# Performance work log

Measured on AMD Instinct MI355X. Metric: run time of the kernel, lower is better.

The kernel has to match this reference:

```python
import jax, jax.numpy as jnp
import numpy as np

B, L, D, H, I = 4, 1024, 2048, 16, 8192
DH = D // H  # 128
EPS = 1e-6


def setup_inputs() -> dict:
    key = jax.random.key(0)
    ks = jax.random.split(key, 10)
    hidden_states = jax.random.normal(ks[0], (B, L, D), dtype=jnp.float32)
    # additive causal mask [B,1,L,L]: 0 on allowed, large negative on masked
    causal = jnp.tril(jnp.ones((L, L), dtype=bool))
    attention_mask = jnp.where(causal, 0.0, -1e9).astype(jnp.float32)
    attention_mask = jnp.broadcast_to(attention_mask[None, None], (B, 1, L, L))
    # RoPE tables [B,L,DH]
    inv_freq = 1.0 / (10000.0 ** (jnp.arange(0, DH, 2, dtype=jnp.float32) / DH))
    pos = jnp.arange(L, dtype=jnp.float32)
    freqs = pos[:, None] * inv_freq[None, :]            # [L, DH/2]
    emb = jnp.concatenate([freqs, freqs], axis=-1)       # [L, DH]
    cos = jnp.broadcast_to(jnp.cos(emb)[None], (B, L, DH)).astype(jnp.float32)
    sin = jnp.broadcast_to(jnp.sin(emb)[None], (B, L, DH)).astype(jnp.float32)
    s = 0.02
    return {
        "hidden_states": hidden_states,
        "attention_mask": attention_mask,
        "cos": cos,
        "sin": sin,
        "q_w": jax.random.normal(ks[1], (D, D), jnp.float32) * s,
        "k_w": jax.random.normal(ks[2], (D, D), jnp.float32) * s,
        "v_w": jax.random.normal(ks[3], (D, D), jnp.float32) * s,
        "o_w": jax.random.normal(ks[4], (D, D), jnp.float32) * s,
        "gate_w": jax.random.normal(ks[5], (I, D), jnp.float32) * s,
        "up_w": jax.random.normal(ks[6], (I, D), jnp.float32) * s,
        "down_w": jax.random.normal(ks[7], (D, I), jnp.float32) * s,
        "ln1_w": jnp.ones((D,), jnp.float32),
        "ln2_w": jnp.ones((D,), jnp.float32),
    }


def _rms_norm(x, w):
    var = jnp.mean(jnp.square(x), axis=-1, keepdims=True)
    return x * jax.lax.rsqrt(var + EPS) * w


def _rotate_half(x):
    x1, x2 = jnp.split(x, 2, axis=-1)
    return jnp.concatenate([-x2, x1], axis=-1)


def reference(hidden_states, attention_mask, cos, sin, q_w, k_w, v_w, o_w,
              gate_w, up_w, down_w, ln1_w, ln2_w):
    residual = hidden_states
    h = _rms_norm(hidden_states, ln1_w)                       # [B,L,D]
    # QKV projections (torch Linear: x @ W^T)
    def heads(x, w):
        return (x @ w.T).reshape(B, L, H, DH).transpose(0, 2, 1, 3)  # [B,H,L,DH]
    q, k, v = heads(h, q_w), heads(h, k_w), heads(h, v_w)
    cos_b, sin_b = cos[:, None], sin[:, None]                 # [B,1,L,DH]
    q = q * cos_b + _rotate_half(q) * sin_b
    k = k * cos_b + _rotate_half(k) * sin_b
    scores = jnp.einsum('bhqd,bhkd->bhqk', q, k) / jnp.sqrt(jnp.float32(DH))
    scores = scores + attention_mask                          # [B,H,L,L]
    attn = jax.nn.softmax(scores, axis=-1)
    ctx = jnp.einsum('bhqk,bhkd->bhqd', attn, v)              # [B,H,L,DH]
    ctx = ctx.transpose(0, 2, 1, 3).reshape(B, L, D)
    attn_out = ctx @ o_w.T
    h1 = residual + attn_out
    h2 = _rms_norm(h1, ln2_w)
    mlp = (jax.nn.silu(h2 @ gate_w.T) * (h2 @ up_w.T)) @ down_w.T
    out = h1 + mlp
    return out, attn
```

## Files before the change

kernel.cpp:

```cpp
#include <hip/hip_runtime.h>


typedef __bf16 bf16;
typedef __bf16 bf16x8 __attribute__((ext_vector_type(8)));
typedef __bf16 bf16x4 __attribute__((ext_vector_type(4)));
typedef float  f32x4  __attribute__((ext_vector_type(4)));

constexpr int   kB  = 4;
constexpr int   kL  = 1024;
constexpr int   kD  = 2048;
constexpr int   kH  = 16;
constexpr int   kI  = 8192;
constexpr int   kDH = 128;
constexpr int   kQKV = 3 * kD;
constexpr float kEps = 1e-6f;
constexpr float kScoreScale = 0.08838834764831845f;

typedef __attribute__((address_space(1))) void gvoid_t;
typedef __attribute__((address_space(3))) void lvoid_t;

__device__ __forceinline__ void gload_lds16(const void* g, void* l) {
  __builtin_amdgcn_global_load_lds((gvoid_t*)g, (lvoid_t*)l, 16, 0, 0);
}

#define ASM_VMCNT(n) asm volatile("s_waitcnt vmcnt(" #n ")" ::: "memory")

__device__ __forceinline__ void bar_raw() {
  asm volatile("" ::: "memory");
  __builtin_amdgcn_s_barrier();
  asm volatile("" ::: "memory");
}

__global__ __launch_bounds__(256) void cast_f32_bf16_kernel(
    const float* __restrict__ x, bf16* __restrict__ y, long n) {
  long i = ((long)blockIdx.x * 256 + threadIdx.x) * 4;
  long stride = (long)gridDim.x * 256 * 4;
  for (; i < n; i += stride) {
    const float4 v = *reinterpret_cast<const float4*>(x + i);
    bf16x4 o;
    o[0] = (bf16)v.x; o[1] = (bf16)v.y; o[2] = (bf16)v.z; o[3] = (bf16)v.w;
    *reinterpret_cast<bf16x4*>(y + i) = o;
  }
}

__global__ __launch_bounds__(256) void add_inplace_kernel(
    float* __restrict__ o, const float* __restrict__ p, long n) {
  long i = ((long)blockIdx.x * 256 + threadIdx.x) * 4;
  const long stride = (long)gridDim.x * 1024;
  for (; i < n; i += stride) {
    float4 a = *(float4*)(o + i);
    const float4 b = *(const float4*)(p + i);
    a.x += b.x; a.y += b.y; a.z += b.z; a.w += b.w;
    *(float4*)(o + i) = a;
  }
}

__global__ __launch_bounds__(256) void rmsnorm_kernel(
    const float* __restrict__ x, const float* __restrict__ w,
    bf16* __restrict__ out) {
  const long row = blockIdx.x;
  const float* xr = x + row * (long)kD;
  bf16* orow = out + row * (long)kD;
  const int t = threadIdx.x;

  float4 v0 = *(const float4*)(xr + t * 8);
  float4 v1 = *(const float4*)(xr + t * 8 + 4);
  float ss = v0.x * v0.x + v0.y * v0.y + v0.z * v0.z + v0.w * v0.w +
             v1.x * v1.x + v1.y * v1.y + v1.z * v1.z + v1.w * v1.w;

  __shared__ float red[4];
  for (int off = 32; off > 0; off >>= 1) ss += __shfl_down(ss, off);
  if ((t & 63) == 0) red[t >> 6] = ss;
  __syncthreads();
  const float tot = red[0] + red[1] + red[2] + red[3];
  const float rs = rsqrtf(tot / (float)kD + kEps);

  float4 w0 = *(const float4*)(w + t * 8);
  float4 w1 = *(const float4*)(w + t * 8 + 4);
  bf16x8 o;
  o[0] = (bf16)(v0.x * rs * w0.x); o[1] = (bf16)(v0.y * rs * w0.y);
  o[2] = (bf16)(v0.z * rs * w0.z); o[3] = (bf16)(v0.w * rs * w0.w);
  o[4] = (bf16)(v1.x * rs * w1.x); o[5] = (bf16)(v1.y * rs * w1.y);
  o[6] = (bf16)(v1.z * rs * w1.z); o[7] = (bf16)(v1.w * rs * w1.w);
  *(bf16x8*)(orow + t * 8) = o;
}

__global__ __launch_bounds__(256) void rope_kernel(
    bf16* __restrict__ qkv, const float* __restrict__ cosb,
    const float* __restrict__ sinb) {
  const long row = blockIdx.x;
  const float* cr = cosb + row * (long)kDH;
  const float* sr = sinb + row * (long)kDH;
  bf16* qr = qkv + row * (long)kQKV;
  bf16* kr = qr + kD;
  const int t = threadIdx.x;
#pragma unroll
  for (int it = 0; it < 4; ++it) {
    const int p = it * 256 + t;
    const int h = p >> 6, i = p & 63;
    const int i0 = h * kDH + i, i1 = i0 + 64;
    const float c0 = cr[i], s0 = sr[i], c1 = cr[i + 64], s1 = sr[i + 64];
    const float q0 = (float)qr[i0], q1 = (float)qr[i1];
    qr[i0] = (bf16)(q0 * c0 - q1 * s0);
    qr[i1] = (bf16)(q1 * c1 + q0 * s1);
    const float k0 = (float)kr[i0], k1 = (float)kr[i1];
    kr[i0] = (bf16)(k0 * c0 - k1 * s0);
    kr[i1] = (bf16)(k1 * c1 + k0 * s1);
  }
}

__global__ __launch_bounds__(256) void transpose_v_kernel(
    const bf16* __restrict__ qkv, bf16* __restrict__ vT) {
  __shared__ bf16 tile[32][33];
  const int z = blockIdx.z, b = z / kH, h = z % kH;
  const bf16* src = qkv + (long)b * kL * kQKV + 2 * kD + h * kDH;
  bf16* dst = vT + (long)z * kDH * kL;
  const int l0 = blockIdx.x * 32, d0 = blockIdx.y * 32;
  const int tx = threadIdx.x & 31, ty = threadIdx.x >> 5;
  for (int r = ty; r < 32; r += 8)
    tile[r][tx] = src[(long)(l0 + r) * kQKV + d0 + tx];
  __syncthreads();
  for (int r = ty; r < 32; r += 8)
    dst[(long)(d0 + r) * kL + l0 + tx] = tile[tx][r];
}

__global__ __launch_bounds__(256) void merge_stats_kernel(
    const float2* __restrict__ sp, float2* __restrict__ sm) {
  const int idx = blockIdx.x * 256 + threadIdx.x;
  const int row = idx & 1023;
  const int n = ((row >> 7) + 1) * 2;
  const float2* p = sp + ((long)idx << 4);
  float M = -3.0e38f;
  for (int i = 0; i < n; ++i) M = fmaxf(M, p[i].x);
  float S = 0.f;
  for (int i = 0; i < n; ++i) S += p[i].y * expf(p[i].x - M);
  sm[idx] = make_float2(M, 1.0f / S);
}

template <int EPI>
__global__ __launch_bounds__(512) void gemm8p(
    const bf16* __restrict__ A, int lda, const bf16* __restrict__ B, int ldb,
    bf16* __restrict__ C, int ldc, const bf16* __restrict__ Ep, int lde,
    int K) {
  __shared__ __align__(16) bf16 ls[2][2][2][128 * 64];
  const int t = threadIdx.x;
  const int m0 = blockIdx.x * 256, n0 = blockIdx.y * 256;
  const int wave = t >> 6, lane = t & 63;
  const int ah = wave >> 2;
  const int wm = ah * 128;
  const int wn = (wave & 3) * 64;
  const int bh = wn >> 7;
  const int wnr = wn & 127;
  const int lr = lane & 15, lg = lane >> 4;

  f32x4 acc[8][4] = {};

  auto stageHalf = [&](int b, int O, int h, int k0) {
    const bf16* S = O ? B : A;
    const int ld = O ? ldb : lda;
    const int base = O ? n0 : m0;
#pragma unroll
    for (int cc = 0; cc < 2; ++cc) {
      const int id = cc * 512 + t;
      const int row = id >> 3, cS = id & 7;
      const int cG = cS ^ (row & 7);
      gload_lds16(S + (long)(base + h * 128 + row) * ld + k0 + cG * 8,
                  (char*)&ls[b][O][h][0] + id * 16);
    }
  };

  auto lread = [&](int b, int O, int h, int row, int c16) {
    return *(const bf16x8*)((const char*)&ls[b][O][h][0] + row * 128 +
                            ((c16 ^ (row & 7)) << 4));
  };

  const int T = K >> 6;
  stageHalf(0, 0, 0, 0); stageHalf(0, 0, 1, 0);
  stageHalf(0, 1, 0, 0); stageHalf(0, 1, 1, 0);
  stageHalf(1, 1, 0, 64); stageHalf(1, 1, 1, 64);

  bf16x8 bfr[2][4];

  for (int w = 0; w < T; ++w) {
    const int c = w & 1;
    const int k1 = (w + 1) << 6, k2 = (w + 2) << 6;
#pragma unroll
    for (int p = 0; p < 4; ++p) {
      bf16x8 af[2][2];
      if (p == 0) {
        if (w + 1 < T) { ASM_VMCNT(4); } else { ASM_VMCNT(0); }
        bar_raw();
#pragma unroll
        for (int kk = 0; kk < 2; ++kk)
#pragma unroll
          for (int nf = 0; nf < 4; ++nf)
            bfr[kk][nf] = lread(c, 1, bh, wnr + nf * 16 + lr, kk * 4 + lg);
      }
#pragma unroll
      for (int kk = 0; kk < 2; ++kk)
#pragma unroll
        for (int mf = 0; mf < 2; ++mf)
          af[kk][mf] = lread(c, 0, ah, (2 * p + mf) * 16 + lr, kk * 4 + lg);
      if (p == 0 && w + 1 < T) stageHalf(c ^ 1, 0, 0, k1);
      if (p == 1 && w + 1 < T) stageHalf(c ^ 1, 0, 1, k1);
      if (p == 2 && w + 2 < T) stageHalf(c, 1, 0, k2);
      if (p == 3 && w + 2 < T) stageHalf(c, 1, 1, k2);
      bar_raw();
      asm volatile("s_waitcnt lgkmcnt(0)" ::: "memory");
      __builtin_amdgcn_sched_barrier(0);
      __builtin_amdgcn_s_setprio(1);
#pragma unroll
      for (int kk = 0; kk < 2; ++kk)
#pragma unroll
        for (int mf = 0; mf < 2; ++mf)
#pragma unroll
          for (int nf = 0; nf < 4; ++nf)
            acc[2 * p + mf][nf] = __builtin_amdgcn_mfma_f32_16x16x32_bf16(
                af[kk][mf], bfr[kk][nf], acc[2 * p + mf][nf], 0, 0, 0);
      __builtin_amdgcn_s_setprio(0);
      bar_raw();
    }
  }

#pragma unroll
  for (int mf = 0; mf < 8; ++mf) {
#pragma unroll
    for (int nf = 0; nf < 4; ++nf) {
      const int col = n0 + wn + nf * 16 + lr;
#pragma unroll
      for (int r = 0; r < 4; ++r) {
        const int row = m0 + wm + mf * 16 + lg * 4 + r;
        float val = acc[mf][nf][r];
        if constexpr (EPI == 3) {
          const float g = (float)Ep[(long)row * lde + col];
          val = (g / (1.0f + expf(-g))) * val;
        }
        C[(long)row * ldc + col] = (bf16)val;
      }
    }
  }
}

__global__ __launch_bounds__(512) void gemm8pF(
    const bf16* __restrict__ A, int lda, const bf16* __restrict__ B, int ldb,
    float* __restrict__ C, int ldc, float* __restrict__ Part, int K) {
  __shared__ __align__(16) bf16 ls[2][2][2][128 * 64];
  const int t = threadIdx.x;
  const int m0 = blockIdx.x * 256, n0 = blockIdx.y * 256;
  const long ko = (long)blockIdx.z * K;
  A += ko; B += ko;
  const int wave = t >> 6, lane = t & 63;
  const int ah = wave >> 2;
  const int wm = ah * 128;
  const int wn = (wave & 3) * 64;
  const int bh = wn >> 7;
  const int wnr = wn & 127;
  const int lr = lane & 15, lg = lane >> 4;

  f32x4 acc[8][4] = {};

  auto stageHalf = [&](int b, int O, int h, int k0) {
    const bf16* S = O ? B : A;
    const int ld = O ? ldb : lda;
    const int base = O ? n0 : m0;
#pragma unroll
    for (int cc = 0; cc < 2; ++cc) {
      const int id = cc * 512 + t;
      const int row = id >> 3, cS = id & 7;
      const int cG = cS ^ (row & 7);
      gload_lds16(S + (long)(base + h * 128 + row) * ld + k0 + cG * 8,
                  (char*)&ls[b][O][h][0] + id * 16);
    }
  };
  auto lread = [&](int b, int O, int h, int row, int c16) {
    return *(const bf16x8*)((const char*)&ls[b][O][h][0] + row * 128 +
                            ((c16 ^ (row & 7)) << 4));
  };

  const int T = K >> 6;
  stageHalf(0, 0, 0, 0); stageHalf(0, 0, 1, 0);
  stageHalf(0, 1, 0, 0); stageHalf(0, 1, 1, 0);
  stageHalf(1, 1, 0, 64); stageHalf(1, 1, 1, 64);

  bf16x8 bfr[2][4];
  for (int w = 0; w < T; ++w) {
    const int c = w & 1;
    const int k1 = (w + 1) << 6, k2 = (w + 2) << 6;
#pragma unroll
    for (int p = 0; p < 4; ++p) {
      bf16x8 af[2][2];
      if (p == 0) {
        if (w + 1 < T) { ASM_VMCNT(4); } else { ASM_VMCNT(0); }
        bar_raw();
#pragma unroll
        for (int kk = 0; kk < 2; ++kk)
#pragma unroll
          for (int nf = 0; nf < 4; ++nf)
            bfr[kk][nf] = lread(c, 1, bh, wnr + nf * 16 + lr, kk * 4 + lg);
      }
#pragma unroll
      for (int kk = 0; kk < 2; ++kk)
#pragma unroll
        for (int mf = 0; mf < 2; ++mf)
          af[kk][mf] = lread(c, 0, ah, (2 * p + mf) * 16 + lr, kk * 4 + lg);
      if (p == 0 && w + 1 < T) stageHalf(c ^ 1, 0, 0, k1);
      if (p == 1 && w + 1 < T) stageHalf(c ^ 1, 0, 1, k1);
      if (p == 2 && w + 2 < T) stageHalf(c, 1, 0, k2);
      if (p == 3 && w + 2 < T) stageHalf(c, 1, 1, k2);
      bar_raw();
      asm volatile("s_waitcnt lgkmcnt(0)" ::: "memory");
      __builtin_amdgcn_sched_barrier(0);
      __builtin_amdgcn_s_setprio(1);
#pragma unroll
      for (int kk = 0; kk < 2; ++kk)
#pragma unroll
        for (int mf = 0; mf < 2; ++mf)
#pragma unroll
          for (int nf = 0; nf < 4; ++nf)
            acc[2 * p + mf][nf] = __builtin_amdgcn_mfma_f32_16x16x32_bf16(
                af[kk][mf], bfr[kk][nf], acc[2 * p + mf][nf], 0, 0, 0);
      __builtin_amdgcn_s_setprio(0);
      bar_raw();
    }
  }

  const bool z0 = (blockIdx.z == 0);
#pragma unroll
  for (int mf = 0; mf < 8; ++mf) {
#pragma unroll
    for (int nf = 0; nf < 4; ++nf) {
      const int col = n0 + wn + nf * 16 + lr;
#pragma unroll
      for (int r = 0; r < 4; ++r) {
        const int row = m0 + wm + mf * 16 + lg * 4 + r;
        const long idx = (long)row * ldc + col;
        if (z0) C[idx] = acc[mf][nf][r] + C[idx];
        else    Part[idx] = acc[mf][nf][r];
      }
    }
  }
}

template <int EPIF>
__global__ __launch_bounds__(512) void gemm8pN128(
    const bf16* __restrict__ A, int lda, const bf16* __restrict__ B, int ldb,
    float* __restrict__ C, int ldc, const float* __restrict__ Ef, int lde,
    int K) {
  __shared__ __align__(16) bf16 lsA[2][2][128 * 64];
  __shared__ __align__(16) bf16 lsB[2][128 * 64];
  const int t = threadIdx.x;
  const int m0 = blockIdx.x * 256, n0 = blockIdx.y * 128;
  const int wave = t >> 6, lane = t & 63;
  const int ah = wave >> 2;
  const int wm = ah * 128;
  const int wn = (wave & 3) * 32;
  const int lr = lane & 15, lg = lane >> 4;

  f32x4 acc[8][2] = {};

  auto stageA = [&](int b, int h, int k0) {
#pragma unroll
    for (int cc = 0; cc < 2; ++cc) {
      const int id = cc * 512 + t;
      const int row = id >> 3, cS = id & 7;
      const int cG = cS ^ (row & 7);
      gload_lds16(A + (long)(m0 + h * 128 + row) * lda + k0 + cG * 8,
                  (char*)&lsA[b][h][0] + id * 16);
    }
  };
  auto stageB = [&](int b, int k0) {
#pragma unroll
    for (int cc = 0; cc < 2; ++cc) {
      const int id = cc * 512 + t;
      const int row = id >> 3, cS = id & 7;
      const int cG = cS ^ (row & 7);
      gload_lds16(B + (long)(n0 + row) * ldb + k0 + cG * 8,
                  (char*)&lsB[b][0] + id * 16);
    }
  };
  auto lreadA = [&](int b, int h, int row, int c16) {
    return *(const bf16x8*)((const char*)&lsA[b][h][0] + row * 128 +
                            ((c16 ^ (row & 7)) << 4));
  };
  auto lreadB = [&](int b, int row, int c16) {
    return *(const bf16x8*)((const char*)&lsB[b][0] + row * 128 +
                            ((c16 ^ (row & 7)) << 4));
  };

  const int T = K >> 6;
  stageA(0, 0, 0); stageA(0, 1, 0);
  stageB(0, 0);
  stageB(1, 64);

  bf16x8 bfr[2][2];
  for (int w = 0; w < T; ++w) {
    const int c = w & 1;
    const int k1 = (w + 1) << 6, k2 = (w + 2) << 6;
#pragma unroll
    for (int p = 0; p < 2; ++p) {
      bf16x8 af[2][4];
      if (p == 0) {
        if (w + 1 < T) { ASM_VMCNT(2); } else { ASM_VMCNT(0); }
        bar_raw();
#pragma unroll
        for (int kk = 0; kk < 2; ++kk)
#pragma unroll
          for (int nf = 0; nf < 2; ++nf)
            bfr[kk][nf] = lreadB(c, wn + nf * 16 + lr, kk * 4 + lg);
      }
#pragma unroll
      for (int kk = 0; kk < 2; ++kk)
#pragma unroll
        for (int mf = 0; mf < 4; ++mf)
          af[kk][mf] = lreadA(c, ah, (4 * p + mf) * 16 + lr, kk * 4 + lg);
      if (p == 0 && w + 1 < T) { stageA(c ^ 1, 0, k1); stageA(c ^ 1, 1, k1); }
      if (p == 1 && w + 2 < T) stageB(c, k2);
      bar_raw();
      asm volatile("s_waitcnt lgkmcnt(0)" ::: "memory");
      __builtin_amdgcn_sched_barrier(0);
      __builtin_amdgcn_s_setprio(1);
#pragma unroll
      for (int kk = 0; kk < 2; ++kk)
#pragma unroll
        for (int mf = 0; mf < 4; ++mf)
#pragma unroll
          for (int nf = 0; nf < 2; ++nf)
            acc[4 * p + mf][nf] = __builtin_amdgcn_mfma_f32_16x16x32_bf16(
                af[kk][mf], bfr[kk][nf], acc[4 * p + mf][nf], 0, 0, 0);
      __builtin_amdgcn_s_setprio(0);
      bar_raw();
    }
  }

#pragma unroll
  for (int mf = 0; mf < 8; ++mf) {
#pragma unroll
    for (int nf = 0; nf < 2; ++nf) {
      const int col = n0 + wn + nf * 16 + lr;
#pragma unroll
      for (int r = 0; r < 4; ++r) {
        const int row = m0 + wm + mf * 16 + lg * 4 + r;
        float val = acc[mf][nf][r];
        const long idx = (long)row * ldc + col;
        if constexpr (EPIF == 1) val += Ef[(long)row * lde + col];
        if constexpr (EPIF == 4) val += C[idx];
        C[idx] = val;
      }
    }
  }
}

enum { EPI_NONE = 0, EPI_ADD = 1, EPI_OUTADD = 4, EPI_PASS1 = 6, EPI_PASS2 = 7 };

template <typename OutT, int EPI, bool AF32, int NF, bool CK>
__device__ __forceinline__ void gemm_body(
    const void* __restrict__ Ap, long sAo, long sAi, int lda,
    const bf16* __restrict__ Bp, long sBo, long sBi, int ldb,
    OutT* Cp, long sCo, long sCi, int ldc,
    const void* Ep, long sEo, long sEi, int lde,
    float scale, int Hdiv, int M, int N, int K) {
  constexpr int BN = 32 * NF;
  constexpr int ACH = 512;
  constexpr int BCH = BN * 4;
  static_assert((EPI != EPI_PASS1 && EPI != EPI_PASS2) || NF == 4, "pass NF=4");

  const int z = blockIdx.z;
  const int zo = z / Hdiv, zi = z % Hdiv;

  const bf16* A = nullptr;
  const float* Af = nullptr;
  if constexpr (AF32) Af = (const float*)Ap + zo * sAo + zi * sAi;
  else                A  = (const bf16*)Ap + zo * sAo + zi * sAi;
  const bf16* Bw = Bp + zo * sBo + zi * sBi;
  OutT* C = Cp + zo * sCo + zi * sCi;

  const int t = threadIdx.x;
  const int m0 = blockIdx.y * 128, n0 = blockIdx.x * BN;

  if constexpr (EPI == EPI_PASS1) {
    if (blockIdx.x > blockIdx.y) return;
  }
  if constexpr (EPI == EPI_PASS2) {
    if (blockIdx.x > blockIdx.y) {
      for (int e = t; e < 128 * 32; e += 256) {
        const int row = e >> 5, col = (e & 31) * 4;
        *(float4*)&C[(long)(m0 + row) * ldc + n0 + col] =
            make_float4(0.f, 0.f, 0.f, 0.f);
      }
      return;
    }
  }

  __shared__ __align__(16) bf16 lsA[2][128 * 32];
  __shared__ __align__(16) bf16 lsB[2][BN * 32];

  const int wave = t >> 6, lane = t & 63;
  const int wm = (wave >> 1) * 64, wn = (wave & 1) * (NF * 16);
  const int lr = lane & 15, lg = lane >> 4;

  f32x4 acc[4][NF] = {};

  auto stage = [&](int buf, int k0) {
    if constexpr (AF32) {
#pragma unroll
      for (int c = 0; c < 2; ++c) {
        const int id = c * 256 + t;
        const int row = id >> 2, col = (id & 3) * 8;
        const float* src = Af + (long)(m0 + row) * lda + k0 + col;
        const float4 u0 = *(const float4*)src;
        const float4 u1 = *(const float4*)(src + 4);
        bf16x8 wv;
        wv[0] = (bf16)u0.x; wv[1] = (bf16)u0.y; wv[2] = (bf16)u0.z; wv[3] = (bf16)u0.w;
        wv[4] = (bf16)u1.x; wv[5] = (bf16)u1.y; wv[6] = (bf16)u1.z; wv[7] = (bf16)u1.w;
        *(bf16x8*)&lsA[buf][id * 8] = wv;
        if (NF == 4 || c == 0)
          gload_lds16(Bw + (long)(n0 + row) * ldb + k0 + col, &lsB[buf][id * 8]);
      }
    } else {
#pragma unroll
      for (int c = 0; c < (ACH + BCH) / 256; ++c) {
        const int id = c * 256 + t;
        if (id < ACH) {
          const int row = id >> 2, col = (id & 3) * 8;
          gload_lds16(A + (long)(m0 + row) * lda + k0 + col, &lsA[buf][id * 8]);
        } else {
          const int fid = id - ACH;
          const int row = fid >> 2, col = (fid & 3) * 8;
          gload_lds16(Bw + (long)(n0 + row) * ldb + k0 + col, &lsB[buf][fid * 8]);
        }
      }
    }
  };

  auto compute = [&](int buf) {
    bf16x8 af[4], bfr[NF];
#pragma unroll
    for (int i = 0; i < 4; ++i)
      af[i] = *(const bf16x8*)&lsA[buf][(wm + i * 16 + lr) * 32 + lg * 8];
#pragma unroll
    for (int j = 0; j < NF; ++j)
      bfr[j] = *(const bf16x8*)&lsB[buf][(wn + j * 16 + lr) * 32 + lg * 8];
#pragma unroll
    for (int i = 0; i < 4; ++i)
#pragma unroll
      for (int j = 0; j < NF; ++j)
        acc[i][j] = __builtin_amdgcn_mfma_f32_16x16x32_bf16(af[i], bfr[j],
                                                            acc[i][j], 0, 0, 0);
  };

  const int Klim = CK ? (m0 + 128) : K;
  int cur = 0;

  if constexpr (AF32) {
    stage(0, 0);
    __syncthreads();
    for (int k0 = 0; k0 < Klim - 32; k0 += 32) {
      stage(cur ^ 1, k0 + 32);
      compute(cur);
      __syncthreads();
      cur ^= 1;
    }
    compute(cur);
  } else {
    stage(0, 0);
    for (int k0 = 0; k0 < Klim - 32; k0 += 32) {
      stage(cur ^ 1, k0 + 32);
      if constexpr (NF == 4) ASM_VMCNT(4); else ASM_VMCNT(3);
      bar_raw();
      compute(cur);
      bar_raw();
      cur ^= 1;
    }
    ASM_VMCNT(0);
    bar_raw();
    compute(cur);
  }

  if constexpr (EPI == EPI_PASS1) {
    float2* statsP = (float2*)Ep;
    const int half = wn >> 6, nt = blockIdx.x;
#pragma unroll
    for (int i = 0; i < 4; ++i) {
#pragma unroll
      for (int r = 0; r < 4; ++r) {
        const int rowg = m0 + wm + i * 16 + lg * 4 + r;
        float v[NF];
        float mx = -3.0e38f;
#pragma unroll
        for (int j = 0; j < NF; ++j) {
          const int colg = n0 + wn + j * 16 + lr;
          v[j] = acc[i][j][r] * scale + (colg > rowg ? -1.0e9f : 0.0f);
          mx = fmaxf(mx, v[j]);
        }
        for (int sh = 1; sh <= 8; sh <<= 1) mx = fmaxf(mx, __shfl_xor(mx, sh));
        float s = 0.f;
#pragma unroll
        for (int j = 0; j < NF; ++j) s += expf(v[j] - mx);
        for (int sh = 1; sh <= 8; sh <<= 1) s += __shfl_xor(s, sh);
        if (lr == 0)
          statsP[(((long)(z << 10) + rowg) << 4) + nt * 2 + half] =
              make_float2(mx, s);
      }
    }
  } else if constexpr (EPI == EPI_PASS2) {
    const float2* sm = (const float2*)Ep;
#pragma unroll
    for (int i = 0; i < 4; ++i) {
#pragma unroll
      for (int j = 0; j < NF; ++j) {
        const int colg = n0 + wn + j * 16 + lr;
#pragma unroll
        for (int r = 0; r < 4; ++r) {
          const int rowg = m0 + wm + i * 16 + lg * 4 + r;
          float p = 0.0f;
          if (colg <= rowg) {
            const float2 st = sm[(z << 10) + rowg];
            p = expf(acc[i][j][r] * scale - st.x) * st.y;
          }
          C[(long)rowg * ldc + colg] = (OutT)p;
        }
      }
    }
  } else {
#pragma unroll
    for (int i = 0; i < 4; ++i) {
#pragma unroll
      for (int j = 0; j < NF; ++j) {
        const int col = n0 + wn + j * 16 + lr;
#pragma unroll
        for (int r = 0; r < 4; ++r) {
          const int rowi = m0 + wm + i * 16 + lg * 4 + r;
          C[(long)rowi * ldc + col] = (OutT)(acc[i][j][r] * scale);
        }
      }
    }
  }
}

#define GEMM_ARGS                                                        \
  const void* __restrict__ Ap, long sAo, long sAi, int lda,              \
  const bf16* __restrict__ Bp, long sBo, long sBi, int ldb,              \
  void* Cp, long sCo, long sCi, int ldc,                                 \
  const void* Ep, long sEo, long sEi, int lde,                           \
  float scale, int Hdiv, int M, int N, int K
#define GEMM_PASS Ap, sAo, sAi, lda, Bp, sBo, sBi, ldb, (OUT_T*)Cp, sCo, \
  sCi, ldc, Ep, sEo, sEi, lde, scale, Hdiv, M, N, K

#define DEF_GEMM(NAME, OUT_TY, EPI_V, AF32_V, NF_V, CK_V)                \
  __global__ __launch_bounds__(256) void NAME(GEMM_ARGS) {               \
    using OUT_T = OUT_TY;                                                \
    gemm_body<OUT_T, EPI_V, AF32_V, NF_V, CK_V>(GEMM_PASS);              \
  }

DEF_GEMM(gemm_sc1, float, EPI_PASS1, false, 4, false)
DEF_GEMM(gemm_sc2, float, EPI_PASS2, false, 4, false)
DEF_GEMM(gemm_ctx, bf16,  EPI_NONE,  true,  2, true)

extern "C" void kernel_launch(void* const* d_in, const int* in_sizes, int n_in,
                              void* d_out, int out_size, void* d_ws,
                              size_t ws_size, hipStream_t stream) {
  (void)in_sizes; (void)n_in; (void)out_size; (void)ws_size;

  const float* hidden = (const float*)d_in[0];
  const float* cosb   = (const float*)d_in[2];
  const float* sinb   = (const float*)d_in[3];
  const float* q_w    = (const float*)d_in[4];
  const float* k_w    = (const float*)d_in[5];
  const float* v_w    = (const float*)d_in[6];
  const float* o_w    = (const float*)d_in[7];
  const float* gate_w = (const float*)d_in[8];
  const float* up_w   = (const float*)d_in[9];
  const float* down_w = (const float*)d_in[10];
  const float* ln1    = (const float*)d_in[11];
  const float* ln2    = (const float*)d_in[12];

  float* out  = (float*)d_out;
  float* attn = out + (long)kB * kL * kD;

  bf16* wsb = (bf16*)d_ws;
  long off = 0;
  bf16* WQKV = wsb + off; off += 3L * kD * kD;
  bf16* WO   = wsb + off; off += (long)kD * kD;
  bf16* WBIG = wsb + off; off += (long)kI * kD;
  bf16* HBF  = wsb + off; off += (long)kB * kL * kD;
  bf16* QKV  = wsb + off; off += (long)kB * kL * kQKV;
  bf16* GBUF = wsb + off; off += (long)kB * kL * kI;

  float2* STATS_P = (float2*)HBF;
  float2* STATS_M = STATS_P + (64L * 1024 * 16);
  float*  DPART   = (float*)HBF;

  const long DD = (long)kD * kD;
  const long ID = (long)kI * kD;
  const int  ML = kB * kL;

  cast_f32_bf16_kernel<<<dim3((int)(DD / 1024)), 256, 0, stream>>>(q_w, WQKV, DD);
  cast_f32_bf16_kernel<<<dim3((int)(DD / 1024)), 256, 0, stream>>>(k_w, WQKV + DD, DD);
  cast_f32_bf16_kernel<<<dim3((int)(DD / 1024)), 256, 0, stream>>>(v_w, WQKV + 2 * DD, DD);
  cast_f32_bf16_kernel<<<dim3((int)(DD / 1024)), 256, 0, stream>>>(o_w, WO, DD);

  rmsnorm_kernel<<<ML, 256, 0, stream>>>(hidden, ln1, HBF);

  gemm8p<0><<<dim3(ML / 256, kQKV / 256), 512, 0, stream>>>(
      HBF, kD, WQKV, kD, QKV, kQKV, nullptr, 0, kD);

  rope_kernel<<<ML, 256, 0, stream>>>(QKV, cosb, sinb);

  transpose_v_kernel<<<dim3(kL / 32, kDH / 32, kB * kH), 256, 0, stream>>>(QKV, GBUF);

  gemm_sc1<<<dim3(kL / 128, kL / 128, kB * kH), 256, 0, stream>>>(
      QKV, (long)kL * kQKV, kDH, kQKV,
      QKV + kD, (long)kL * kQKV, kDH, kQKV,
      attn, (long)kH * kL * kL, (long)kL * kL, kL,
      STATS_P, 0, 0, 0,
      kScoreScale, kH, kL, kL, kDH);

  merge_stats_kernel<<<256, 256, 0, stream>>>(STATS_P, STATS_M);

  gemm_sc2<<<dim3(kL / 128, kL / 128, kB * kH), 256, 0, stream>>>(
      QKV, (long)kL * kQKV, kDH, kQKV,
      QKV + kD, (long)kL * kQKV, kDH, kQKV,
      attn, (long)kH * kL * kL, (long)kL * kL, kL,
      STATS_M, 0, 0, 0,
      kScoreScale, kH, kL, kL, kDH);

  gemm_ctx<<<dim3(kDH / 64, kL / 128, kB * kH), 256, 0, stream>>>(
      attn, (long)kH * kL * kL, (long)kL * kL, kL,
      GBUF, (long)kH * kDH * kL, (long)kDH * kL, kL,
      HBF, (long)kL * kD, kDH, kD,
      nullptr, 0, 0, 0, 1.0f, kH, kL, kDH, kL);

  gemm8pN128<1><<<dim3(ML / 256, kD / 128), 512, 0, stream>>>(
      HBF, kD, WO, kD, out, kD, hidden, kD, kD);

  bf16* H2 = QKV;
  rmsnorm_kernel<<<ML, 256, 0, stream>>>(out, ln2, H2);

  cast_f32_bf16_kernel<<<dim3((int)(ID / 1024)), 256, 0, stream>>>(gate_w, WBIG, ID);
  gemm8p<0><<<dim3(ML / 256, kI / 256), 512, 0, stream>>>(
      H2, kD, WBIG, kD, GBUF, kI, nullptr, 0, kD);

  cast_f32_bf16_kernel<<<dim3((int)(ID / 1024)), 256, 0, stream>>>(up_w, WBIG, ID);
  gemm8p<3><<<dim3(ML / 256, kI / 256), 512, 0, stream>>>(
      H2, kD, WBIG, kD, GBUF, kI, GBUF, kI, kD);

  cast_f32_bf16_kernel<<<dim3((int)(ID / 1024)), 256, 0, stream>>>(down_w, WBIG, ID);
  gemm8pF<<<dim3(ML / 256, kD / 256, 2), 512, 0, stream>>>(
      GBUF, kI, WBIG, kI, out, kD, DPART, kI / 2);

  add_inplace_kernel<<<2048, 256, 0, stream>>>(out, DPART, (long)ML * kD);
}
```

Before: 1.010 ms.

## Fuse gate and up GEMMs with SiLU, drop split-K for down projection

A new gemm8pMLP kernel computes the gate and up projections in one pass. Each block stages the activation tile once, accumulates gate and up results side by side, and writes the SiLU-gated product directly. This removes one full GEMM read of the activations and the write and re-read of the intermediate gate buffer. The down projection now uses the existing N128 GEMM with an epilogue variant (EPIF 4) instead of split-K with a partial buffer, so the separate add kernel goes away. The cost is a second bf16 weight buffer in the workspace, and one thread block now carries the whole K=8192 reduction.

```diff
diff --git a/kernel.cpp b/kernel.cpp
--- a/kernel.cpp
+++ b/kernel.cpp
@@ -40,18 +40,6 @@
     bf16x4 o;
     o[0] = (bf16)v.x; o[1] = (bf16)v.y; o[2] = (bf16)v.z; o[3] = (bf16)v.w;
     *reinterpret_cast<bf16x4*>(y + i) = o;
-  }
-}
-
-__global__ __launch_bounds__(256) void add_inplace_kernel(
-    float* __restrict__ o, const float* __restrict__ p, long n) {
-  long i = ((long)blockIdx.x * 256 + threadIdx.x) * 4;
-  const long stride = (long)gridDim.x * 1024;
-  for (; i < n; i += stride) {
-    float4 a = *(float4*)(o + i);
-    const float4 b = *(const float4*)(p + i);
-    a.x += b.x; a.y += b.y; a.z += b.z; a.w += b.w;
-    *(float4*)(o + i) = a;
   }
 }
 
@@ -241,48 +229,54 @@
   }
 }
 
-__global__ __launch_bounds__(512) void gemm8pF(
-    const bf16* __restrict__ A, int lda, const bf16* __restrict__ B, int ldb,
-    float* __restrict__ C, int ldc, float* __restrict__ Part, int K) {
-  __shared__ __align__(16) bf16 ls[2][2][2][128 * 64];
+__global__ __launch_bounds__(512) void gemm8pMLP(
+    const bf16* __restrict__ A, int lda,
+    const bf16* __restrict__ Bg, const bf16* __restrict__ Bu, int ldb,
+    bf16* __restrict__ C, int ldc, int K) {
+  __shared__ __align__(16) bf16 lsA[2][2][128 * 64];
+  __shared__ __align__(16) bf16 lsG[2][128 * 64];
+  __shared__ __align__(16) bf16 lsU[2][128 * 64];
   const int t = threadIdx.x;
-  const int m0 = blockIdx.x * 256, n0 = blockIdx.y * 256;
-  const long ko = (long)blockIdx.z * K;
-  A += ko; B += ko;
+  const int m0 = blockIdx.x * 256, n0 = blockIdx.y * 128;
   const int wave = t >> 6, lane = t & 63;
   const int ah = wave >> 2;
   const int wm = ah * 128;
-  const int wn = (wave & 3) * 64;
-  const int bh = wn >> 7;
-  const int wnr = wn & 127;
+  const int wn = (wave & 3) * 32;
   const int lr = lane & 15, lg = lane >> 4;
 
-  f32x4 acc[8][4] = {};
-
-  auto stageHalf = [&](int b, int O, int h, int k0) {
-    const bf16* S = O ? B : A;
-    const int ld = O ? ldb : lda;
-    const int base = O ? n0 : m0;
+  f32x4 aG[8][2] = {}, aU[8][2] = {};
+
+  auto stageA = [&](int b, int h, int k0) {
 #pragma unroll
     for (int cc = 0; cc < 2; ++cc) {
       const int id = cc * 512 + t;
       const int row = id >> 3, cS = id & 7;
       const int cG = cS ^ (row & 7);
-      gload_lds16(S + (long)(base + h * 128 + row) * ld + k0 + cG * 8,
-                  (char*)&ls[b][O][h][0] + id * 16);
-    }
-  };
-  auto lread = [&](int b, int O, int h, int row, int c16) {
-    return *(const bf16x8*)((const char*)&ls[b][O][h][0] + row * 128 +
+      gload_lds16(A + (long)(m0 + h * 128 + row) * lda + k0 + cG * 8,
+                  (char*)&lsA[b][h][0] + id * 16);
+    }
+  };
+  auto stageW = [&](bf16* dst, const bf16* B, int k0) {
+#pragma unroll
+    for (int cc = 0; cc < 2; ++cc) {
+      const int id = cc * 512 + t;
+      const int row = id >> 3, cS = id & 7;
+      const int cG = cS ^ (row & 7);
+      gload_lds16(B + (long)(n0 + row) * ldb + k0 + cG * 8,
+                  (char*)dst + id * 16);
+    }
+  };
+  auto lread = [&](const bf16* base, int row, int c16) {
+    return *(const bf16x8*)((const char*)base + row * 128 +
                             ((c16 ^ (row & 7)) << 4));
   };
 
   const int T = K >> 6;
-  stageHalf(0, 0, 0, 0); stageHalf(0, 0, 1, 0);
-  stageHalf(0, 1, 0, 0); stageHalf(0, 1, 1, 0);
-  stageHalf(1, 1, 0, 64); stageHalf(1, 1, 1, 64);
-
-  bf16x8 bfr[2][4];
+  stageA(0, 0, 0); stageA(0, 1, 0);
+  stageW(lsG[0], Bg, 0); stageW(lsU[0], Bu, 0);
+  stageW(lsG[1], Bg, 64); stageW(lsU[1], Bu, 64);
+
+  bf16x8 bG[2][2], bU[2][2];
   for (int w = 0; w < T; ++w) {
     const int c = w & 1;
     const int k1 = (w + 1) << 6, k2 = (w + 2) << 6;
@@ -295,18 +289,20 @@
 #pragma unroll
         for (int kk = 0; kk < 2; ++kk)
 #pragma unroll
-          for (int nf = 0; nf < 4; ++nf)
-            bfr[kk][nf] = lread(c, 1, bh, wnr + nf * 16 + lr, kk * 4 + lg);
+          for (int nf = 0; nf < 2; ++nf) {
+            bG[kk][nf] = lread(lsG[c], wn + nf * 16 + lr, kk * 4 + lg);
+            bU[kk][nf] = lread(lsU[c], wn + nf * 16 + lr, kk * 4 + lg);
+          }
       }
 #pragma unroll
       for (int kk = 0; kk < 2; ++kk)
 #pragma unroll
         for (int mf = 0; mf < 2; ++mf)
-          af[kk][mf] = lread(c, 0, ah, (2 * p + mf) * 16 + lr, kk * 4 + lg);
-      if (p == 0 && w + 1 < T) stageHalf(c ^ 1, 0, 0, k1);
-      if (p == 1 && w + 1 < T) stageHalf(c ^ 1, 0, 1, k1);
-      if (p == 2 && w + 2 < T) stageHalf(c, 1, 0, k2);
-      if (p == 3 && w + 2 < T) stageHalf(c, 1, 1, k2);
+          af[kk][mf] = lread(lsA[c][ah], (2 * p + mf) * 16 + lr, kk * 4 + lg);
+      if (p == 0 && w + 1 < T) stageA(c ^ 1, 0, k1);
+      if (p == 1 && w + 1 < T) stageA(c ^ 1, 1, k1);
+      if (p == 2 && w + 2 < T) stageW(lsG[c], Bg, k2);
+      if (p == 3 && w + 2 < T) stageW(lsU[c], Bu, k2);
       bar_raw();
       asm volatile("s_waitcnt lgkmcnt(0)" ::: "memory");
       __builtin_amdgcn_sched_barrier(0);
@@ -316,26 +312,27 @@
 #pragma unroll
         for (int mf = 0; mf < 2; ++mf)
 #pragma unroll
-          for (int nf = 0; nf < 4; ++nf)
-            acc[2 * p + mf][nf] = __builtin_amdgcn_mfma_f32_16x16x32_bf16(
-                af[kk][mf], bfr[kk][nf], acc[2 * p + mf][nf], 0, 0, 0);
+          for (int nf = 0; nf < 2; ++nf) {
+            aG[2 * p + mf][nf] = __builtin_amdgcn_mfma_f32_16x16x32_bf16(
+                af[kk][mf], bG[kk][nf], aG[2 * p + mf][nf], 0, 0, 0);
+            aU[2 * p + mf][nf] = __builtin_amdgcn_mfma_f32_16x16x32_bf16(
+                af[kk][mf], bU[kk][nf], aU[2 * p + mf][nf], 0, 0, 0);
+          }
       __builtin_amdgcn_s_setprio(0);
       bar_raw();
     }
   }
 
-  const bool z0 = (blockIdx.z == 0);
 #pragma unroll
   for (int mf = 0; mf < 8; ++mf) {
 #pragma unroll
-    for (int nf = 0; nf < 4; ++nf) {
+    for (int nf = 0; nf < 2; ++nf) {
       const int col = n0 + wn + nf * 16 + lr;
 #pragma unroll
       for (int r = 0; r < 4; ++r) {
         const int row = m0 + wm + mf * 16 + lg * 4 + r;
-        const long idx = (long)row * ldc + col;
-        if (z0) C[idx] = acc[mf][nf][r] + C[idx];
-        else    Part[idx] = acc[mf][nf][r];
+        const float g = aG[mf][nf][r], u = aU[mf][nf][r];
+        C[(long)row * ldc + col] = (bf16)((g / (1.0f + expf(-g))) * u);
       }
     }
   }
@@ -681,14 +678,14 @@
   long off = 0;
   bf16* WQKV = wsb + off; off += 3L * kD * kD;
   bf16* WO   = wsb + off; off += (long)kD * kD;
-  bf16* WBIG = wsb + off; off += (long)kI * kD;
+  bf16* WG   = wsb + off; off += (long)kI * kD;
+  bf16* WU   = wsb + off; off += (long)kI * kD;
   bf16* HBF  = wsb + off; off += (long)kB * kL * kD;
   bf16* QKV  = wsb + off; off += (long)kB * kL * kQKV;
   bf16* GBUF = wsb + off; off += (long)kB * kL * kI;
 
   float2* STATS_P = (float2*)HBF;
   float2* STATS_M = STATS_P + (64L * 1024 * 16);
-  float*  DPART   = (float*)HBF;
 
   const long DD = (long)kD * kD;
   const long ID = (long)kI * kD;
@@ -736,17 +733,12 @@
   bf16* H2 = QKV;
   rmsnorm_kernel<<<ML, 256, 0, stream>>>(out, ln2, H2);
 
-  cast_f32_bf16_kernel<<<dim3((int)(ID / 1024)), 256, 0, stream>>>(gate_w, WBIG, ID);
-  gemm8p<0><<<dim3(ML / 256, kI / 256), 512, 0, stream>>>(
-      H2, kD, WBIG, kD, GBUF, kI, nullptr, 0, kD);
-
-  cast_f32_bf16_kernel<<<dim3((int)(ID / 1024)), 256, 0, stream>>>(up_w, WBIG, ID);
-  gemm8p<3><<<dim3(ML / 256, kI / 256), 512, 0, stream>>>(
-      H2, kD, WBIG, kD, GBUF, kI, GBUF, kI, kD);
-
-  cast_f32_bf16_kernel<<<dim3((int)(ID / 1024)), 256, 0, stream>>>(down_w, WBIG, ID);
-  gemm8pF<<<dim3(ML / 256, kD / 256, 2), 512, 0, stream>>>(
-      GBUF, kI, WBIG, kI, out, kD, DPART, kI / 2);
-
-  add_inplace_kernel<<<2048, 256, 0, stream>>>(out, DPART, (long)ML * kD);
-}
+  cast_f32_bf16_kernel<<<dim3((int)(ID / 1024)), 256, 0, stream>>>(gate_w, WG, ID);
+  cast_f32_bf16_kernel<<<dim3((int)(ID / 1024)), 256, 0, stream>>>(up_w, WU, ID);
+  gemm8pMLP<<<dim3(ML / 256, kI / 128), 512, 0, stream>>>(
+      H2, kD, WG, WU, kD, GBUF, kI, kD);
+
+  cast_f32_bf16_kernel<<<dim3((int)(ID / 1024)), 256, 0, stream>>>(down_w, WG, ID);
+  gemm8pN128<4><<<dim3(ML / 256, kD / 128), 512, 0, stream>>>(
+      GBUF, kI, WG, kI, out, kD, nullptr, 0, kI);
+}
```

New measurement: 969.2 us. 4.0% less time.
